# Optimization experiments

Measured on AMD Instinct MI355X. Metric: run time of the kernel, lower is better.

Reference implementation:

```python
import jax, jax.numpy as jnp
import numpy as np

H = 256          # hidden_dim
K = 5            # num_mixtures
Z = 32           # latent_dim
A = 3            # action dim
B, T = 128, 512
IN = Z + A       # LSTM input features
MDN = K * (1 + 2 * Z)  # 325


def setup_inputs() -> dict:
    key = jax.random.key(0)
    ks = jax.random.split(key, 8)
    s_in = 1.0 / np.sqrt(IN)
    s_h = 1.0 / np.sqrt(H)
    return {
        "z_t": jax.random.normal(ks[0], (B, T, Z), jnp.float32),
        "a_t": jax.random.normal(ks[1], (B, T, A), jnp.float32),
        # LSTM params: fused gate kernels, gate order [i, f, g, o]
        "Wx": jax.random.normal(ks[2], (IN, 4 * H), jnp.float32) * s_in,
        "Wh": jax.random.normal(ks[3], (H, 4 * H), jnp.float32) * s_h,
        "b": jnp.zeros((4 * H,), jnp.float32),
        # MDN head Dense(325)
        "Wd": jax.random.normal(ks[4], (H, MDN), jnp.float32) * s_h,
        "bd": jnp.zeros((MDN,), jnp.float32),
    }


def _mdnrnn(z_t, a_t, Wx, Wh, b, Wd, bd):
    x = jnp.concatenate([z_t, a_t], axis=-1)          # (B,T,IN)
    # hoist the input projection out of the recurrence (same math)
    xproj = jnp.einsum("bti,ig->btg", x, Wx)          # (B,T,4H)
    xproj_t = jnp.swapaxes(xproj, 0, 1)               # (T,B,4H)
    bsz = x.shape[0]
    c0 = jnp.zeros((bsz, H), x.dtype)
    h0 = jnp.zeros((bsz, H), x.dtype)

    def step(carry, xp):
        c, h = carry
        gates = xp + h @ Wh + b                        # (B,4H)
        i, f, g, o = jnp.split(gates, 4, axis=-1)
        i = jax.nn.sigmoid(i)
        f = jax.nn.sigmoid(f)
        g = jnp.tanh(g)
        o = jax.nn.sigmoid(o)
        c = f * c + i * g
        h = o * jnp.tanh(c)
        return (c, h), h

    final_carry, hs = jax.lax.scan(step, (c0, h0), xproj_t)
    outputs = jnp.swapaxes(hs, 0, 1)                  # (B,T,H)

    mdn = outputs @ Wd + bd                           # (B,T,325)
    log_pi, mu, log_sigma = jnp.split(mdn, [K, K + K * Z * 2 // 2 + K * Z - K], axis=-1)
    # splits: [K, (1+Z)*K] -> log_pi (K), mu (K*Z), log_sigma (K*Z)
    log_pi, mu, log_sigma = mdn[..., :K], mdn[..., K:K + K * Z], mdn[..., K + K * Z:]
    bt = outputs.shape[:2]
    mu = mu.reshape(bt[0], bt[1], K, Z)
    log_sigma = log_sigma.reshape(bt[0], bt[1], K, Z)
    log_pi = jax.nn.log_softmax(log_pi, axis=-1)
    sigma = jnp.exp(log_sigma) + 1e-06
    return log_pi, mu, sigma, final_carry


def reference(z_t, a_t, Wx, Wh, b, Wd, bd):
    return _mdnrnn(z_t, a_t, Wx, Wh, b, Wd, bd)
```

## Files before the change

### kernel.cpp

```cpp
#include <hip/hip_runtime.h>
#include <hip/hip_bf16.h>
#include <math.h>

#define T_LEN 512
#define B_SZ  128
#define H_DIM 256
#define G_DIM 1024
#define IN_D  35
#define MDN_D 325
#define K_MIX 5

#define NSLICE 4
#define BG     2
#define NGRP   64

static constexpr long OFF_MU    = 327680L;
static constexpr long OFF_SIGMA = 10813440L;
static constexpr long OFF_C     = 21299200L;
static constexpr long OFF_H     = 21331968L;

static constexpr size_t WS_OUT = 0;
static constexpr size_t WS_HG  = 33554432;

typedef unsigned uint2v  __attribute__((ext_vector_type(2)));
typedef float    float2v __attribute__((ext_vector_type(2)));
typedef float    float4v __attribute__((ext_vector_type(4)));

__device__ __forceinline__ float fast_sigmoid(float x) { return 1.0f / (1.0f + __expf(-x)); }
__device__ __forceinline__ float fast_tanh(float x) {
    return 1.0f - 2.0f / (__expf(2.0f * x) + 1.0f);
}

__device__ __forceinline__ void pk_fma_lo(float2v& acc, float2v w, float2v h) {
    asm("v_pk_fma_f32 %0, %1, %2, %0 op_sel:[0,0,0] op_sel_hi:[1,0,1]"
        : "+v"(acc) : "v"(w), "v"(h));
}
__device__ __forceinline__ void pk_fma_hi(float2v& acc, float2v w, float2v h) {
    asm("v_pk_fma_f32 %0, %1, %2, %0 op_sel:[0,1,0] op_sel_hi:[1,1,1]"
        : "+v"(acc) : "v"(w), "v"(h));
}

__global__ __launch_bounds__(512, 1) void lstm6_kernel(
    const float* __restrict__ z_t, const float* __restrict__ a_t,
    const float* __restrict__ Wx,  const float* __restrict__ Wh,
    const float* __restrict__ bias,
    float* __restrict__ h_glb,
    __hip_bfloat16* __restrict__ outs,
    float* __restrict__ out_c, float* __restrict__ out_h)
{
    const int bid = blockIdx.x;
    const int gr  = bid & 63;
    const int s   = bid >> 6;
    const int tid = threadIdx.x;
    const int cg  = tid >> 2;
    const int kq  = tid & 3;
    const int lc0 = cg * 2;
    const int gate = lc0 >> 6;
    const int j0   = lc0 & 63;
    const int gcol0 = gate * 256 + s * 64 + j0;

    __shared__ __align__(16) float h_lds[BG][4][68];
    __shared__ __align__(16) float x_lds[BG][44];
    __shared__ __align__(16) float g_red[BG][256];

    for (int i = tid; i < BG * 4 * 68; i += 512) ((float*)h_lds)[i] = 0.0f;
    if (tid < BG * 9) { int b = tid / 9, k = tid - 9 * b; x_lds[b][35 + k] = 0.0f; }

    float2v W2[64];
    #pragma unroll
    for (int i = 0; i < 64; ++i) {
        const size_t r = (size_t)(kq * 64 + i) * G_DIM;
        W2[i].x = Wh[r + gcol0];
        W2[i].y = Wh[r + gcol0 + 1];
    }
    float2v X2[10];
    #pragma unroll
    for (int i = 0; i < 10; ++i) {
        int xk = kq * 10 + i;
        bool ok = (xk < IN_D);
        X2[i].x = ok ? Wx[(size_t)xk * G_DIM + gcol0]     : 0.0f;
        X2[i].y = ok ? Wx[(size_t)xk * G_DIM + gcol0 + 1] : 0.0f;
    }
    #pragma unroll
    for (int i = 0; i < 64; ++i) asm volatile("" : "+v"(W2[i]));
    #pragma unroll
    for (int i = 0; i < 10; ++i) asm volatile("" : "+v"(X2[i]));

    const int cb = tid >> 6;
    const int cj = tid & 63;
    const float bc0 = bias[0 * 256 + s * 64 + cj];
    const float bc1 = bias[1 * 256 + s * 64 + cj];
    const float bc2 = bias[2 * 256 + s * 64 + cj];
    const float bc3 = bias[3 * 256 + s * 64 + cj];
    float c_reg = 0.0f;

    const int q  = tid - 128;
    const int pb = (q >= 96) ? 1 : 0;
    const int pp = q - 96 * pb;
    const int pk0 = pp * 2;
    const int pkk = pk0 + ((pk0 >= s * 64) ? 64 : 0);

    const int batch0 = gr * BG;
    float* hg = h_glb + (size_t)gr * (2 * BG * H_DIM);

    if (tid >= 384 && tid < 448) {
        int qq = tid - 384, b = qq >> 5, k = qq & 31;
        x_lds[b][k] = z_t[((size_t)(batch0 + b) * T_LEN + 0) * 32 + k];
    } else if (tid >= 448 && tid < 448 + BG * 3) {
        int qq = tid - 448, b = (qq >= 3), k = qq - 3 * b;
        x_lds[b][32 + k] = a_t[((size_t)(batch0 + b) * T_LEN + 0) * 3 + k];
    }
    __syncthreads();

    for (int t = 0; t < T_LEN; ++t) {
        if (t > 0 && tid >= 128 && tid < 320) {
            const unsigned want = (unsigned)((t - 1) & 3);
            const float* ap = hg + ((t - 1) & 1) * (BG * H_DIM) + pb * H_DIM + pkk;
            uint2v u;
            do {
                asm volatile("global_load_dwordx2 %0, %1, off sc0 sc1\n\t"
                             "s_waitcnt vmcnt(0)"
                             : "=v"(u) : "v"(ap) : "memory");
            } while ((u.x & 3u) != want || (u.y & 3u) != want);
            float* dst = &h_lds[pb][pkk >> 6][pkk & 63];
            dst[0] = __uint_as_float(u.x);
            dst[1] = __uint_as_float(u.y);
        }
        __syncthreads();

        float2v acc0 = {0.0f, 0.0f}, acc1 = {0.0f, 0.0f};
        {
            const float4v* hp0 = (const float4v*)h_lds[0][kq];
            const float4v* hp1 = (const float4v*)h_lds[1][kq];
            #pragma unroll
            for (int i4 = 0; i4 < 16; ++i4) {
                float4v hv0 = hp0[i4];
                float4v hv1 = hp1[i4];
                float2v h0lo = __builtin_shufflevector(hv0, hv0, 0, 1);
                float2v h0hi = __builtin_shufflevector(hv0, hv0, 2, 3);
                float2v h1lo = __builtin_shufflevector(hv1, hv1, 0, 1);
                float2v h1hi = __builtin_shufflevector(hv1, hv1, 2, 3);
                pk_fma_lo(acc0, W2[4*i4+0], h0lo); pk_fma_lo(acc1, W2[4*i4+0], h1lo);
                pk_fma_hi(acc0, W2[4*i4+1], h0lo); pk_fma_hi(acc1, W2[4*i4+1], h1lo);
                pk_fma_lo(acc0, W2[4*i4+2], h0hi); pk_fma_lo(acc1, W2[4*i4+2], h1hi);
                pk_fma_hi(acc0, W2[4*i4+3], h0hi); pk_fma_hi(acc1, W2[4*i4+3], h1hi);
            }
            #pragma unroll
            for (int i = 0; i < 5; ++i) {
                float2v xv0 = *(const float2v*)&x_lds[0][kq * 10 + 2 * i];
                float2v xv1 = *(const float2v*)&x_lds[1][kq * 10 + 2 * i];
                pk_fma_lo(acc0, X2[2*i],   xv0); pk_fma_lo(acc1, X2[2*i],   xv1);
                pk_fma_hi(acc0, X2[2*i+1], xv0); pk_fma_hi(acc1, X2[2*i+1], xv1);
            }
        }
        float a00 = acc0.x, a01 = acc0.y, a10 = acc1.x, a11 = acc1.y;
        a00 += __shfl_xor(a00, 1, 64); a00 += __shfl_xor(a00, 2, 64);
        a01 += __shfl_xor(a01, 1, 64); a01 += __shfl_xor(a01, 2, 64);
        a10 += __shfl_xor(a10, 1, 64); a10 += __shfl_xor(a10, 2, 64);
        a11 += __shfl_xor(a11, 1, 64); a11 += __shfl_xor(a11, 2, 64);
        if (kq == 0) {
            g_red[0][lc0] = a00; g_red[0][lc0 + 1] = a01;
            g_red[1][lc0] = a10; g_red[1][lc0 + 1] = a11;
        }
        __syncthreads();

        if (tid < 128) {
            float gi = g_red[cb][      cj] + bc0;
            float gf = g_red[cb][ 64 + cj] + bc1;
            float gg = g_red[cb][128 + cj] + bc2;
            float go = g_red[cb][192 + cj] + bc3;
            float iv = fast_sigmoid(gi), fv = fast_sigmoid(gf), ov = fast_sigmoid(go);
            float gv = fast_tanh(gg);
            c_reg = fmaf(fv, c_reg, iv * gv);
            float hv = ov * fast_tanh(c_reg);
            unsigned u = (__float_as_uint(hv) & ~3u) | (unsigned)(t & 3);
            float* dst = hg + (t & 1) * (BG * H_DIM) + cb * H_DIM + s * 64 + cj;
            asm volatile("global_store_dword %0, %1, off sc0 sc1"
                         :: "v"(dst), "v"(u) : "memory");
            h_lds[cb][s][cj] = __uint_as_float(u);
            outs[((size_t)(batch0 + cb) * T_LEN + t) * H_DIM + s * 64 + cj] =
                __float2bfloat16(hv);
            if (t == T_LEN - 1) {
                out_c[(batch0 + cb) * H_DIM + s * 64 + cj] = c_reg;
                out_h[(batch0 + cb) * H_DIM + s * 64 + cj] = hv;
            }
        }
        if (t + 1 < T_LEN) {
            if (tid >= 384 && tid < 448) {
                int qq = tid - 384, b = qq >> 5, k = qq & 31;
                x_lds[b][k] = z_t[((size_t)(batch0 + b) * T_LEN + (t + 1)) * 32 + k];
            } else if (tid >= 448 && tid < 448 + BG * 3) {
                int qq = tid - 448, b = (qq >= 3), k = qq - 3 * b;
                x_lds[b][32 + k] = a_t[((size_t)(batch0 + b) * T_LEN + (t + 1)) * 3 + k];
            }
        }
    }
}

__global__ __launch_bounds__(256, 1) void mdn_kernel(
    const unsigned short* __restrict__ outputs, const float* __restrict__ Wd,
    const float* __restrict__ bd, float* __restrict__ out)
{
    __shared__ __align__(16) float hT[H_DIM * 16];
    __shared__ float lp[16][K_MIX];

    const int tid = threadIdx.x;
    const long row0 = (long)blockIdx.x * 16;

    for (int idx = tid; idx < H_DIM * 16; idx += 256) {
        int r = idx >> 8;
        int k = idx & (H_DIM - 1);
        unsigned int u = outputs[(row0 + r) * H_DIM + k];
        hT[k * 16 + r] = __uint_as_float(u << 16);
    }
    __syncthreads();

    const int  cA = tid;
    const int  cB = tid + 256;
    const bool vB = (cB < MDN_D);
    const float bA = bd[cA];
    const float bB = vB ? bd[cB] : 0.0f;
    float accA[16], accB[16];
    #pragma unroll
    for (int r = 0; r < 16; ++r) { accA[r] = bA; accB[r] = bB; }

    for (int k = 0; k < H_DIM; ++k) {
        float wA = Wd[(size_t)k * MDN_D + cA];
        float wB = vB ? Wd[(size_t)k * MDN_D + cB] : 0.0f;
        const float4* hp = (const float4*)(hT + k * 16);
        float4 h0 = hp[0], h1 = hp[1], h2 = hp[2], h3 = hp[3];
        float hr[16] = { h0.x,h0.y,h0.z,h0.w, h1.x,h1.y,h1.z,h1.w,
                         h2.x,h2.y,h2.z,h2.w, h3.x,h3.y,h3.z,h3.w };
        #pragma unroll
        for (int r = 0; r < 16; ++r) {
            accA[r] = fmaf(hr[r], wA, accA[r]);
            accB[r] = fmaf(hr[r], wB, accB[r]);
        }
    }

    float* out_mu = out + OFF_MU;
    float* out_sg = out + OFF_SIGMA;
    #pragma unroll
    for (int r = 0; r < 16; ++r) {
        long row = row0 + r;
        float v = accA[r];
        if (cA < K_MIX)            lp[r][cA] = v;
        else if (cA < K_MIX + 160) out_mu[row * 160 + (cA - K_MIX)] = v;
        else                       out_sg[row * 160 + (cA - 165)]   = __expf(v) + 1e-6f;
        if (vB)                    out_sg[row * 160 + (cB - 165)]   = __expf(accB[r]) + 1e-6f;
    }
    __syncthreads();

    if (tid < 16) {
        int r = tid;
        long row = row0 + r;
        float v0 = lp[r][0], v1 = lp[r][1], v2 = lp[r][2], v3 = lp[r][3], v4 = lp[r][4];
        float m = fmaxf(fmaxf(fmaxf(v0, v1), fmaxf(v2, v3)), v4);
        float sum = __expf(v0-m) + __expf(v1-m) + __expf(v2-m) + __expf(v3-m) + __expf(v4-m);
        float ls = m + __logf(sum);
        out[row*5 + 0] = v0 - ls;
        out[row*5 + 1] = v1 - ls;
        out[row*5 + 2] = v2 - ls;
        out[row*5 + 3] = v3 - ls;
        out[row*5 + 4] = v4 - ls;
    }
}

extern "C" void kernel_launch(void* const* d_in, const int* in_sizes, int n_in,
                              void* d_out, int out_size, void* d_ws, size_t ws_size,
                              hipStream_t stream)
{
    const float* z_t = (const float*)d_in[0];
    const float* a_t = (const float*)d_in[1];
    const float* Wx  = (const float*)d_in[2];
    const float* Wh  = (const float*)d_in[3];
    const float* b   = (const float*)d_in[4];
    const float* Wd  = (const float*)d_in[5];
    const float* bd  = (const float*)d_in[6];
    float* out = (float*)d_out;

    char* ws = (char*)d_ws;
    __hip_bfloat16* outs = (__hip_bfloat16*)(ws + WS_OUT);
    float* h_glb         = (float*)(ws + WS_HG);

    lstm6_kernel<<<NGRP * NSLICE, 512, 0, stream>>>(z_t, a_t, Wx, Wh, b,
                                                    h_glb, outs,
                                                    out + OFF_C, out + OFF_H);
    mdn_kernel<<<(B_SZ * T_LEN) / 16, 256, 0, stream>>>((const unsigned short*)outs,
                                                        Wd, bd, out);
}
```

Measured before the change: 1.192 ms.

## Stagger two batch rows in LSTM so one's exchange overlaps other's matvec

Each block still owns two batch rows, but the two are now processed in alternating half-steps rather than together. While the matvec for row A runs, the cross-block h exchange for row B is already in flight, and the reverse for the other half. Input x loads are also prefetched two steps ahead into registers. The aim is to hide the global-memory spin-wait latency of the inter-block h exchange behind compute. The cost is twice as many block barriers per timestep, each matvec carrying half the work, and more complex synchronisation.

```diff
diff --git a/kernel.cpp b/kernel.cpp
--- a/kernel.cpp
+++ b/kernel.cpp
@@ -11,7 +11,6 @@
 #define K_MIX 5
 
 #define NSLICE 4
-#define BG     2
 #define NGRP   64
 
 static constexpr long OFF_MU    = 327680L;
@@ -22,9 +21,8 @@
 static constexpr size_t WS_OUT = 0;
 static constexpr size_t WS_HG  = 33554432;
 
-typedef unsigned uint2v  __attribute__((ext_vector_type(2)));
-typedef float    float2v __attribute__((ext_vector_type(2)));
-typedef float    float4v __attribute__((ext_vector_type(4)));
+typedef float float2v __attribute__((ext_vector_type(2)));
+typedef float float4v __attribute__((ext_vector_type(4)));
 
 __device__ __forceinline__ float fast_sigmoid(float x) { return 1.0f / (1.0f + __expf(-x)); }
 __device__ __forceinline__ float fast_tanh(float x) {
@@ -40,7 +38,7 @@
         : "+v"(acc) : "v"(w), "v"(h));
 }
 
-__global__ __launch_bounds__(512, 1) void lstm6_kernel(
+__global__ __launch_bounds__(512, 1) void lstm11_kernel(
     const float* __restrict__ z_t, const float* __restrict__ a_t,
     const float* __restrict__ Wx,  const float* __restrict__ Wh,
     const float* __restrict__ bias,
@@ -59,12 +57,14 @@
     const int j0   = lc0 & 63;
     const int gcol0 = gate * 256 + s * 64 + j0;
 
-    __shared__ __align__(16) float h_lds[BG][4][68];
-    __shared__ __align__(16) float x_lds[BG][44];
-    __shared__ __align__(16) float g_red[BG][256];
-
-    for (int i = tid; i < BG * 4 * 68; i += 512) ((float*)h_lds)[i] = 0.0f;
-    if (tid < BG * 9) { int b = tid / 9, k = tid - 9 * b; x_lds[b][35 + k] = 0.0f; }
+    __shared__ __align__(16) float hC[2][4][68];
+    __shared__ __align__(16) float xA[44];
+    __shared__ __align__(16) float xB2[2][44];
+    __shared__ __align__(16) float gA[256], gB[256];
+
+    for (int i = tid; i < 2 * 4 * 68; i += 512) ((float*)hC)[i] = 0.0f;
+    if (tid < 44) xA[tid] = 0.0f;
+    if (tid >= 64 && tid < 152) ((float*)xB2)[tid - 64] = 0.0f;
 
     float2v W2[64];
     #pragma unroll
@@ -86,112 +86,185 @@
     #pragma unroll
     for (int i = 0; i < 10; ++i) asm volatile("" : "+v"(X2[i]));
 
-    const int cb = tid >> 6;
-    const int cj = tid & 63;
-    const float bc0 = bias[0 * 256 + s * 64 + cj];
-    const float bc1 = bias[1 * 256 + s * 64 + cj];
-    const float bc2 = bias[2 * 256 + s * 64 + cj];
-    const float bc3 = bias[3 * 256 + s * 64 + cj];
+    const int wj = tid & 63;
+    float bc0 = 0, bc1 = 0, bc2 = 0, bc3 = 0;
+    if (tid < 128) {
+        bc0 = bias[0 * 256 + s * 64 + wj];
+        bc1 = bias[1 * 256 + s * 64 + wj];
+        bc2 = bias[2 * 256 + s * 64 + wj];
+        bc3 = bias[3 * 256 + s * 64 + wj];
+    }
     float c_reg = 0.0f;
 
-    const int q  = tid - 128;
-    const int pb = (q >= 96) ? 1 : 0;
-    const int pp = q - 96 * pb;
-    const int pk0 = pp * 2;
-    const int pkk = pk0 + ((pk0 >= s * 64) ? 64 : 0);
-
-    const int batch0 = gr * BG;
-    float* hg = h_glb + (size_t)gr * (2 * BG * H_DIM);
-
-    if (tid >= 384 && tid < 448) {
-        int qq = tid - 384, b = qq >> 5, k = qq & 31;
-        x_lds[b][k] = z_t[((size_t)(batch0 + b) * T_LEN + 0) * 32 + k];
-    } else if (tid >= 448 && tid < 448 + BG * 3) {
-        int qq = tid - 448, b = (qq >= 3), k = qq - 3 * b;
-        x_lds[b][32 + k] = a_t[((size_t)(batch0 + b) * T_LEN + 0) * 3 + k];
+    const bool isp = (tid >= 128 && tid < 320);
+    const int  pp  = tid - 128;
+    const int  pkk = pp + ((pp >= s * 64) ? 64 : 0);
+    unsigned pA = 0, pB = 0;
+
+    const int  sq    = tid - 384;
+    const bool is_st = (sq >= 0 && sq < 2 * IN_D);
+    const int  sb    = (sq >= IN_D) ? 1 : 0;
+    const int  sk    = sq - IN_D * sb;
+    float xv_next = 0.0f;
+
+    const int batch0 = gr * 2;
+    float* hg  = h_glb + (size_t)gr * 1024;
+    float* hgA = hg;
+    float* hgB = hg + 512;
+
+    if (is_st) {
+        const size_t rb = (size_t)(batch0 + sb) * T_LEN;
+        float v0 = (sk < 32) ? z_t[(rb + 0) * 32 + sk] : a_t[(rb + 0) * 3 + (sk - 32)];
+        if (sb == 0) xA[sk] = v0; else xB2[0][sk] = v0;
+        xv_next = (sk < 32) ? z_t[(rb + 1) * 32 + sk] : a_t[(rb + 1) * 3 + (sk - 32)];
     }
     __syncthreads();
 
     for (int t = 0; t < T_LEN; ++t) {
-        if (t > 0 && tid >= 128 && tid < 320) {
+        if (t > 0 && isp) {
             const unsigned want = (unsigned)((t - 1) & 3);
-            const float* ap = hg + ((t - 1) & 1) * (BG * H_DIM) + pb * H_DIM + pkk;
-            uint2v u;
-            do {
-                asm volatile("global_load_dwordx2 %0, %1, off sc0 sc1\n\t"
-                             "s_waitcnt vmcnt(0)"
-                             : "=v"(u) : "v"(ap) : "memory");
-            } while ((u.x & 3u) != want || (u.y & 3u) != want);
-            float* dst = &h_lds[pb][pkk >> 6][pkk & 63];
-            dst[0] = __uint_as_float(u.x);
-            dst[1] = __uint_as_float(u.y);
+            asm volatile("s_waitcnt vmcnt(0)" : "+v"(pA) :: "memory");
+            if ((pA & 3u) != want) {
+                const float* ap = hgA + ((t - 1) & 1) * 256 + pkk;
+                do {
+                    asm volatile("global_load_dword %0, %1, off sc0 sc1\n\t"
+                                 "s_waitcnt vmcnt(0)"
+                                 : "=v"(pA) : "v"(ap) : "memory");
+                } while ((pA & 3u) != want);
+            }
+            hC[0][pkk >> 6][pkk & 63] = __uint_as_float(pA);
         }
         __syncthreads();
 
-        float2v acc0 = {0.0f, 0.0f}, acc1 = {0.0f, 0.0f};
+        float xv_new = 0.0f;
+        if (is_st && t + 2 < T_LEN) {
+            const size_t rb = (size_t)(batch0 + sb) * T_LEN;
+            xv_new = (sk < 32) ? z_t[(rb + t + 2) * 32 + sk]
+                               : a_t[(rb + t + 2) * 3 + (sk - 32)];
+        }
+
+        float2v acc = {0.0f, 0.0f};
         {
-            const float4v* hp0 = (const float4v*)h_lds[0][kq];
-            const float4v* hp1 = (const float4v*)h_lds[1][kq];
+            const float4v* hp = (const float4v*)hC[0][kq];
             #pragma unroll
             for (int i4 = 0; i4 < 16; ++i4) {
-                float4v hv0 = hp0[i4];
-                float4v hv1 = hp1[i4];
-                float2v h0lo = __builtin_shufflevector(hv0, hv0, 0, 1);
-                float2v h0hi = __builtin_shufflevector(hv0, hv0, 2, 3);
-                float2v h1lo = __builtin_shufflevector(hv1, hv1, 0, 1);
-                float2v h1hi = __builtin_shufflevector(hv1, hv1, 2, 3);
-                pk_fma_lo(acc0, W2[4*i4+0], h0lo); pk_fma_lo(acc1, W2[4*i4+0], h1lo);
-                pk_fma_hi(acc0, W2[4*i4+1], h0lo); pk_fma_hi(acc1, W2[4*i4+1], h1lo);
-                pk_fma_lo(acc0, W2[4*i4+2], h0hi); pk_fma_lo(acc1, W2[4*i4+2], h1hi);
-                pk_fma_hi(acc0, W2[4*i4+3], h0hi); pk_fma_hi(acc1, W2[4*i4+3], h1hi);
+                float4v hv = hp[i4];
+                float2v lo = __builtin_shufflevector(hv, hv, 0, 1);
+                float2v hi = __builtin_shufflevector(hv, hv, 2, 3);
+                pk_fma_lo(acc, W2[4*i4+0], lo);
+                pk_fma_hi(acc, W2[4*i4+1], lo);
+                pk_fma_lo(acc, W2[4*i4+2], hi);
+                pk_fma_hi(acc, W2[4*i4+3], hi);
+            }
+            if (isp && t > 0) {
+                const float* ap = hgB + ((t - 1) & 1) * 256 + pkk;
+                asm volatile("global_load_dword %0, %1, off sc0 sc1"
+                             : "=v"(pB) : "v"(ap) : "memory");
             }
             #pragma unroll
             for (int i = 0; i < 5; ++i) {
-                float2v xv0 = *(const float2v*)&x_lds[0][kq * 10 + 2 * i];
-                float2v xv1 = *(const float2v*)&x_lds[1][kq * 10 + 2 * i];
-                pk_fma_lo(acc0, X2[2*i],   xv0); pk_fma_lo(acc1, X2[2*i],   xv1);
-                pk_fma_hi(acc0, X2[2*i+1], xv0); pk_fma_hi(acc1, X2[2*i+1], xv1);
-            }
-        }
-        float a00 = acc0.x, a01 = acc0.y, a10 = acc1.x, a11 = acc1.y;
-        a00 += __shfl_xor(a00, 1, 64); a00 += __shfl_xor(a00, 2, 64);
-        a01 += __shfl_xor(a01, 1, 64); a01 += __shfl_xor(a01, 2, 64);
-        a10 += __shfl_xor(a10, 1, 64); a10 += __shfl_xor(a10, 2, 64);
-        a11 += __shfl_xor(a11, 1, 64); a11 += __shfl_xor(a11, 2, 64);
-        if (kq == 0) {
-            g_red[0][lc0] = a00; g_red[0][lc0 + 1] = a01;
-            g_red[1][lc0] = a10; g_red[1][lc0 + 1] = a11;
+                float2v xv = *(const float2v*)&xA[kq * 10 + 2 * i];
+                pk_fma_lo(acc, X2[2*i],   xv);
+                pk_fma_hi(acc, X2[2*i+1], xv);
+            }
+        }
+        {
+            float a0 = acc.x, a1 = acc.y;
+            a0 += __shfl_xor(a0, 1, 64); a0 += __shfl_xor(a0, 2, 64);
+            a1 += __shfl_xor(a1, 1, 64); a1 += __shfl_xor(a1, 2, 64);
+            if (kq == 0) { gA[lc0] = a0; gA[lc0 + 1] = a1; }
         }
         __syncthreads();
 
-        if (tid < 128) {
-            float gi = g_red[cb][      cj] + bc0;
-            float gf = g_red[cb][ 64 + cj] + bc1;
-            float gg = g_red[cb][128 + cj] + bc2;
-            float go = g_red[cb][192 + cj] + bc3;
+        if (tid < 64) {
+            float gi = gA[wj] + bc0, gf = gA[64 + wj] + bc1;
+            float gg = gA[128 + wj] + bc2, go = gA[192 + wj] + bc3;
             float iv = fast_sigmoid(gi), fv = fast_sigmoid(gf), ov = fast_sigmoid(go);
             float gv = fast_tanh(gg);
             c_reg = fmaf(fv, c_reg, iv * gv);
             float hv = ov * fast_tanh(c_reg);
             unsigned u = (__float_as_uint(hv) & ~3u) | (unsigned)(t & 3);
-            float* dst = hg + (t & 1) * (BG * H_DIM) + cb * H_DIM + s * 64 + cj;
+            float* dst = hgA + (t & 1) * 256 + s * 64 + wj;
             asm volatile("global_store_dword %0, %1, off sc0 sc1"
                          :: "v"(dst), "v"(u) : "memory");
-            h_lds[cb][s][cj] = __uint_as_float(u);
-            outs[((size_t)(batch0 + cb) * T_LEN + t) * H_DIM + s * 64 + cj] =
+            hC[0][s][wj] = __uint_as_float(u);
+            outs[((size_t)batch0 * T_LEN + t) * H_DIM + s * 64 + wj] = __float2bfloat16(hv);
+            if (t == T_LEN - 1) {
+                out_c[batch0 * H_DIM + s * 64 + wj] = c_reg;
+                out_h[batch0 * H_DIM + s * 64 + wj] = hv;
+            }
+        }
+        if (isp && t > 0) {
+            const unsigned want = (unsigned)((t - 1) & 3);
+            asm volatile("s_waitcnt vmcnt(0)" : "+v"(pB) :: "memory");
+            if ((pB & 3u) != want) {
+                const float* ap = hgB + ((t - 1) & 1) * 256 + pkk;
+                do {
+                    asm volatile("global_load_dword %0, %1, off sc0 sc1\n\t"
+                                 "s_waitcnt vmcnt(0)"
+                                 : "=v"(pB) : "v"(ap) : "memory");
+                } while ((pB & 3u) != want);
+            }
+            hC[1][pkk >> 6][pkk & 63] = __uint_as_float(pB);
+        }
+        if (is_st && t + 1 < T_LEN) {
+            if (sb == 0) xA[sk] = xv_next;
+            else         xB2[(t + 1) & 1][sk] = xv_next;
+            xv_next = xv_new;
+        }
+        __syncthreads();
+
+        acc.x = 0.0f; acc.y = 0.0f;
+        {
+            const float4v* hp = (const float4v*)hC[1][kq];
+            #pragma unroll
+            for (int i4 = 0; i4 < 16; ++i4) {
+                float4v hv = hp[i4];
+                float2v lo = __builtin_shufflevector(hv, hv, 0, 1);
+                float2v hi = __builtin_shufflevector(hv, hv, 2, 3);
+                pk_fma_lo(acc, W2[4*i4+0], lo);
+                pk_fma_hi(acc, W2[4*i4+1], lo);
+                pk_fma_lo(acc, W2[4*i4+2], hi);
+                pk_fma_hi(acc, W2[4*i4+3], hi);
+            }
+            if (isp) {
+                const float* ap = hgA + (t & 1) * 256 + pkk;
+                asm volatile("global_load_dword %0, %1, off sc0 sc1"
+                             : "=v"(pA) : "v"(ap) : "memory");
+            }
+            const float* xb = xB2[t & 1];
+            #pragma unroll
+            for (int i = 0; i < 5; ++i) {
+                float2v xv = *(const float2v*)&xb[kq * 10 + 2 * i];
+                pk_fma_lo(acc, X2[2*i],   xv);
+                pk_fma_hi(acc, X2[2*i+1], xv);
+            }
+        }
+        {
+            float a0 = acc.x, a1 = acc.y;
+            a0 += __shfl_xor(a0, 1, 64); a0 += __shfl_xor(a0, 2, 64);
+            a1 += __shfl_xor(a1, 1, 64); a1 += __shfl_xor(a1, 2, 64);
+            if (kq == 0) { gB[lc0] = a0; gB[lc0 + 1] = a1; }
+        }
+        __syncthreads();
+
+        if (tid >= 64 && tid < 128) {
+            float gi = gB[wj] + bc0, gf = gB[64 + wj] + bc1;
+            float gg = gB[128 + wj] + bc2, go = gB[192 + wj] + bc3;
+            float iv = fast_sigmoid(gi), fv = fast_sigmoid(gf), ov = fast_sigmoid(go);
+            float gv = fast_tanh(gg);
+            c_reg = fmaf(fv, c_reg, iv * gv);
+            float hv = ov * fast_tanh(c_reg);
+            unsigned u = (__float_as_uint(hv) & ~3u) | (unsigned)(t & 3);
+            float* dst = hgB + (t & 1) * 256 + s * 64 + wj;
+            asm volatile("global_store_dword %0, %1, off sc0 sc1"
+                         :: "v"(dst), "v"(u) : "memory");
+            hC[1][s][wj] = __uint_as_float(u);
+            outs[((size_t)(batch0 + 1) * T_LEN + t) * H_DIM + s * 64 + wj] =
                 __float2bfloat16(hv);
             if (t == T_LEN - 1) {
-                out_c[(batch0 + cb) * H_DIM + s * 64 + cj] = c_reg;
-                out_h[(batch0 + cb) * H_DIM + s * 64 + cj] = hv;
-            }
-        }
-        if (t + 1 < T_LEN) {
-            if (tid >= 384 && tid < 448) {
-                int qq = tid - 384, b = qq >> 5, k = qq & 31;
-                x_lds[b][k] = z_t[((size_t)(batch0 + b) * T_LEN + (t + 1)) * 32 + k];
-            } else if (tid >= 448 && tid < 448 + BG * 3) {
-                int qq = tid - 448, b = (qq >= 3), k = qq - 3 * b;
-                x_lds[b][32 + k] = a_t[((size_t)(batch0 + b) * T_LEN + (t + 1)) * 3 + k];
+                out_c[(batch0 + 1) * H_DIM + s * 64 + wj] = c_reg;
+                out_h[(batch0 + 1) * H_DIM + s * 64 + wj] = hv;
             }
         }
     }
@@ -283,9 +356,9 @@
     __hip_bfloat16* outs = (__hip_bfloat16*)(ws + WS_OUT);
     float* h_glb         = (float*)(ws + WS_HG);
 
-    lstm6_kernel<<<NGRP * NSLICE, 512, 0, stream>>>(z_t, a_t, Wx, Wh, b,
-                                                    h_glb, outs,
-                                                    out + OFF_C, out + OFF_H);
+    lstm11_kernel<<<NGRP * NSLICE, 512, 0, stream>>>(z_t, a_t, Wx, Wh, b,
+                                                     h_glb, outs,
+                                                     out + OFF_C, out + OFF_H);
     mdn_kernel<<<(B_SZ * T_LEN) / 16, 256, 0, stream>>>((const unsigned short*)outs,
                                                         Wd, bd, out);
 }
```

New measurement: 1.255 ms. 5.3% more time.
